# Performance work log

Hardware: AMD Instinct MI355X
Metric: run time of the kernel (lower is better)

The kernel has to match this reference:

```python
import jax, jax.numpy as jnp
import numpy as np

B, L, D, H = 2, 2048, 2048, 16
HD = D // H          # head_dim = 128
LAT = HD // 4        # latent_dim = 32


def setup_inputs() -> dict:
    key = jax.random.key(0)
    ks = jax.random.split(key, 16)
    def w(k, shape, fan_in):
        return jax.random.normal(k, shape, jnp.float32) / np.float32(np.sqrt(fan_in))
    x = jax.random.normal(ks[0], (B, L, D), jnp.float32)
    # RoPE frequencies, stored as (cos, sin) pairs: [L, HD//2, 2]
    inv_freq = 1.0 / (10000.0 ** (np.arange(0, HD, 2, dtype=np.float32) / HD))
    ang = np.outer(np.arange(L, dtype=np.float32), inv_freq)
    freqs_cis = jnp.stack([jnp.asarray(np.cos(ang)), jnp.asarray(np.sin(ang))], axis=-1)
    return dict(
        x=x, freqs_cis=freqs_cis,
        Wq=w(ks[1], (D, D), D), bq=jnp.zeros((D,), jnp.float32),
        Wk=w(ks[2], (D, D), D), bk=jnp.zeros((D,), jnp.float32),
        Wv=w(ks[3], (D, D), D), bv=jnp.zeros((D,), jnp.float32),
        Wqc=w(ks[4], (LAT, HD), HD), bqc=jnp.zeros((LAT,), jnp.float32),
        Wkc=w(ks[5], (LAT, HD), HD), bkc=jnp.zeros((LAT,), jnp.float32),
        Wvc=w(ks[6], (LAT, HD), HD), bvc=jnp.zeros((LAT,), jnp.float32),
        Wd=w(ks[7], (HD, LAT), LAT), bd=jnp.zeros((HD,), jnp.float32),
        Wo=w(ks[8], (D, D), D), bo=jnp.zeros((D,), jnp.float32),
    )


def _rope(t, freqs_cis):
    # t: [B,H,L,HD]; freqs_cis: [L, HD//2, 2] (cos, sin)
    tp = t.reshape(t.shape[:-1] + (HD // 2, 2))
    a, b = tp[..., 0], tp[..., 1]
    cr = freqs_cis[:, :, 0]  # [L, HD//2]
    ci = freqs_cis[:, :, 1]
    ra = a * cr - b * ci
    rb = a * ci + b * cr
    return jnp.stack([ra, rb], axis=-1).reshape(t.shape)


def reference(x, freqs_cis, Wq, bq, Wk, bk, Wv, bv, Wqc, bqc, Wkc, bkc, Wvc, bvc, Wd, bd, Wo, bo):
    Bx, Lx, Dx = x.shape
    # QKV projections -> [B,H,L,HD]
    def proj(W, bias):
        return (x @ W.T + bias).reshape(Bx, Lx, H, HD).transpose(0, 2, 1, 3)
    q = proj(Wq, bq)
    k = proj(Wk, bk)
    v = proj(Wv, bv)
    q = _rope(q, freqs_cis)
    k = _rope(k, freqs_cis)
    # per-head compression to latent dim: [B,H,L,LAT]
    qc = q @ Wqc.T + bqc
    kc = k @ Wkc.T + bkc
    vc = v @ Wvc.T + bvc
    scores = jnp.einsum('bhie,bhje->bhij', qc, kc) / np.float32(np.sqrt(LAT))
    mask = jnp.triu(jnp.ones((Lx, Lx), bool), 1)  # future positions
    scores = jnp.where(mask, jnp.float32(-jnp.inf), scores)
    probs = jax.nn.softmax(scores, axis=-1)
    attn = jnp.einsum('bhij,bhje->bhie', probs, vc)  # [B,H,L,LAT]
    attn = attn @ Wd.T + bd                          # decompress -> [B,H,L,HD]
    attn = attn.transpose(0, 2, 1, 3).reshape(Bx, Lx, Dx)
    return attn @ Wo.T + bo
```

## Files before the change

kernel.cpp:

```cpp
#include <hip/hip_runtime.h>

typedef __attribute__((ext_vector_type(8))) __bf16 bf16x8;
typedef __attribute__((ext_vector_type(4))) __bf16 bf16x4;
typedef __attribute__((ext_vector_type(4))) float f32x4;
typedef __attribute__((ext_vector_type(16))) float f32x16;

#define LL 2048
#define DD 2048
#define HH 16
#define HDIM 128

__global__ __launch_bounds__(256)
void setup_all(const float* __restrict__ x, const float* __restrict__ Wq,
               const float* __restrict__ Wk, const float* __restrict__ Wqc,
               const float* __restrict__ Wkc,
               const float* __restrict__ Wv, const float* __restrict__ Wvc,
               const float* __restrict__ bv, const float* __restrict__ bvc,
               const float* __restrict__ Wo, const float* __restrict__ Wd,
               const float* __restrict__ bd, const float* __restrict__ bo,
               __bf16* __restrict__ xb, __bf16* __restrict__ Wqb, __bf16* __restrict__ Wkb,
               __bf16* __restrict__ Wqcb, __bf16* __restrict__ Wkcb,
               __bf16* __restrict__ Wveff, float* __restrict__ bveff,
               __bf16* __restrict__ Woeff, float* __restrict__ boeff)
{
    __shared__ float sm[128 * 32];
    const int tid = threadIdx.x;
    const int bid = blockIdx.x;

    if (bid < 16392) {
        size_t i = (size_t)bid * 256 + tid;
        const float* s; __bf16* d; size_t off;
        if (i < 2097152)      { s = x;   d = xb;   off = i; }
        else if (i < 3145728) { s = Wq;  d = Wqb;  off = i - 2097152; }
        else if (i < 4194304) { s = Wk;  d = Wkb;  off = i - 3145728; }
        else if (i < 4195328) { s = Wqc; d = Wqcb; off = i - 4194304; }
        else                  { s = Wkc; d = Wkcb; off = i - 4195328; }
        float4 v = *(const float4*)(s + off * 4);
        bf16x4 o = { (__bf16)v.x, (__bf16)v.y, (__bf16)v.z, (__bf16)v.w };
        *(bf16x4*)(d + off * 4) = o;
        return;
    }
    int idx = bid - 16392;
    if (idx < 512) {
        float (*WvcT)[32] = (float(*)[32])sm;
        const int h = idx >> 5, dc = idx & 31;
        for (int i = tid; i < 4096; i += 256) WvcT[i & 127][i >> 7] = Wvc[i];
        __syncthreads();
        const int d  = dc * 64 + (tid & 63);
        const int o0 = (tid >> 6) * 8;
        float acc[8] = {};
        for (int jj = 0; jj < 128; ++jj) {
            const float w = Wv[(size_t)(h * 128 + jj) * 2048 + d];
            #pragma unroll
            for (int o = 0; o < 8; ++o) acc[o] += WvcT[jj][o0 + o] * w;
        }
        #pragma unroll
        for (int o = 0; o < 8; ++o)
            Wveff[(size_t)(h * 32 + o0 + o) * 2048 + d] = (__bf16)acc[o];
        if (dc == 0 && tid < 32) {
            float s = bvc[tid];
            for (int jj = 0; jj < 128; ++jj) s += WvcT[jj][tid] * bv[h * 128 + jj];
            bveff[h * 32 + tid] = s;
        }
        return;
    }
    idx -= 512;
    if (idx < 512) {
        float (*WdL)[32] = (float(*)[32])sm;
        const int dc = idx & 31, h = idx >> 5;
        for (int i = tid; i < 4096; i += 256) WdL[i >> 5][i & 31] = Wd[i];
        __syncthreads();
        const int dout = dc * 64 + (tid & 63);
        const int o0   = (tid >> 6) * 8;
        float acc[8] = {};
        const float* wrow = Wo + (size_t)dout * 2048 + h * 128;
        for (int u = 0; u < 128; ++u) {
            const float w = wrow[u];
            #pragma unroll
            for (int o = 0; o < 8; ++o) acc[o] += WdL[u][o0 + o] * w;
        }
        #pragma unroll
        for (int o = 0; o < 8; ++o)
            Woeff[(size_t)dout * 512 + h * 32 + o0 + o] = (__bf16)acc[o];
        return;
    }
    idx -= 512;
    float* bdL = sm;
    if (tid < 128) bdL[tid] = bd[tid];
    __syncthreads();
    const int d  = idx * 32 + (tid >> 3);
    const int s0 = (tid & 7) * 64;
    float s = 0.f;
    const float* wrow = Wo + (size_t)d * 2048 + s0 * 4;
    for (int c4 = 0; c4 < 64; ++c4) {
        float4 wv = *(const float4*)(wrow + c4 * 4);
        const int cb = ((s0 + c4) * 4) & 127;
        s += wv.x * bdL[cb] + wv.y * bdL[cb + 1] + wv.z * bdL[cb + 2] + wv.w * bdL[cb + 3];
    }
    #pragma unroll
    for (int off = 4; off; off >>= 1) s += __shfl_down(s, off, 8);
    if ((tid & 7) == 0) boeff[d] = bo[d] + s;
}

typedef unsigned int u32;
typedef const __attribute__((address_space(1))) u32* gp_t;
typedef __attribute__((address_space(3))) u32* lp_t;
__device__ __forceinline__ void gload16(const __bf16* g, __bf16* l)
{
    __builtin_amdgcn_global_load_lds((gp_t)(const void*)g, (lp_t)(void*)l, 16, 0, 0);
}

#define MF16(a, b, c) __builtin_amdgcn_mfma_f32_16x16x32_bf16(a, b, c, 0, 0, 0)

__global__ __launch_bounds__(256, 2)
void gemm_qkv(const __bf16* __restrict__ A,
              const __bf16* __restrict__ Wq, const __bf16* __restrict__ Wk,
              const __bf16* __restrict__ Wveff,
              const float* __restrict__ bq, const float* __restrict__ bk,
              const float* __restrict__ bveff,
              const __bf16* __restrict__ Wqcb, const __bf16* __restrict__ Wkcb,
              const float* __restrict__ bqc, const float* __restrict__ bkc,
              const float* __restrict__ fc,
              __bf16* __restrict__ qc, __bf16* __restrict__ kc, __bf16* __restrict__ vt)
{
    __shared__ __bf16 lds[3][12288];

    const int bid = blockIdx.x;
    const int xcd = bid & 7;
    const int j   = bid >> 3;
    const int bx  = j >> 2;
    const int byl = j & 3;
    const int by  = xcd * 4 + byl;
    const int m0  = by * 128;
    const int which = (bx >= 16) ? 2 : (bx >> 3);
    const int n0  = (which == 2) ? (bx - 16) * 256 : (bx & 7) * 256;
    const __bf16* W = which == 0 ? Wq : which == 1 ? Wk : Wveff;

    const int tid  = threadIdx.x;
    const int wid  = tid >> 6;
    const int lane = tid & 63;
    const int wr   = wid >> 1;
    const int wc   = wid & 1;
    const int l15  = lane & 15;
    const int l4   = lane >> 4;
    const int swz  = (l4 ^ (l15 & 3) ^ ((l15 >> 2) & 3)) * 8;

    const int srl  = lane >> 2;
    const int scol = ((lane & 3) ^ (srl & 3) ^ ((srl >> 2) & 3)) * 8;
    const __bf16* gA0 = A + (size_t)(m0 + wid * 32 + srl) * 2048 + scol;
    const __bf16* gB0 = W + (size_t)(n0 + wid * 64 + srl) * 2048 + scol;

    #define STAGE(bb, kk)                                                \
    {   __bf16* dA = &lds[bb][wid * 1024];                               \
        __bf16* dB = &lds[bb][4096 + wid * 2048];                        \
        gload16(gA0 + (kk), dA);                                         \
        gload16(gA0 + (size_t)16 * 2048 + (kk), dA + 512);               \
        gload16(gB0 + (kk), dB);                                         \
        gload16(gB0 + (size_t)16 * 2048 + (kk), dB + 512);               \
        gload16(gB0 + (size_t)32 * 2048 + (kk), dB + 1024);              \
        gload16(gB0 + (size_t)48 * 2048 + (kk), dB + 1536);              \
    }
    #define RD_A(bb, mf) (*(const bf16x8*)&lds[bb][(wr * 64 + (mf) * 16 + l15) * 32 + swz])
    #define RD_B(bb, nf) (*(const bf16x8*)&lds[bb][4096 + (wc * 128 + (nf) * 16 + l15) * 32 + swz])

    f32x4 acc[4][8] = {};

    STAGE(0, 0) STAGE(1, 32)
    asm volatile("s_waitcnt vmcnt(6)" ::: "memory");
    __builtin_amdgcn_s_barrier();

    #define TB(RB, SB, VM, DOST, kk)                                          \
    {                                                                         \
        bf16x8 fa[4], fb[8];                                                  \
        fa[0] = RD_A(RB, 0); fa[1] = RD_A(RB, 1);                             \
        fa[2] = RD_A(RB, 2); fa[3] = RD_A(RB, 3);                             \
        fb[0] = RD_B(RB, 0); fb[1] = RD_B(RB, 1);                             \
        fb[2] = RD_B(RB, 2); fb[3] = RD_B(RB, 3);                             \
        fb[4] = RD_B(RB, 4); fb[5] = RD_B(RB, 5);                             \
        fb[6] = RD_B(RB, 6); fb[7] = RD_B(RB, 7);                             \
        if (DOST) STAGE(SB, kk)                                               \
        asm volatile("s_waitcnt lgkmcnt(0)" ::: "memory");                    \
        __builtin_amdgcn_sched_barrier(0);                                    \
        __builtin_amdgcn_s_setprio(1);                                        \
        _Pragma("unroll")                                                     \
        for (int mf = 0; mf < 4; ++mf)                                        \
            _Pragma("unroll")                                                 \
            for (int nf = 0; nf < 8; ++nf)                                    \
                acc[mf][nf] = MF16(fa[mf], fb[nf], acc[mf][nf]);              \
        __builtin_amdgcn_s_setprio(0);                                        \
        asm volatile("s_waitcnt vmcnt(" VM ")" ::: "memory");                 \
        __builtin_amdgcn_s_barrier();                                         \
    }

    for (int tt = 0; tt < 60; tt += 3) {
        const int kk = (tt + 2) * 32;
        TB(0, 2, "6", true, kk)
        TB(1, 0, "6", true, kk + 32)
        TB(2, 1, "6", true, kk + 64)
    }
    TB(0, 2, "6", true, 62 * 32)
    TB(1, 0, "6", true, 63 * 32)
    TB(2, 0, "0", false, 0)
    TB(0, 0, "0", false, 0)
    #undef TB
    #undef STAGE
    #undef RD_A
    #undef RD_B

    if (which < 2) {
        __bf16* qt = &lds[0][0];
        const float* bb_ = which ? bk : bq;
        const __bf16* Wb = which ? Wkcb : Wqcb;
        const float*  bs = which ? bkc : bqc;
        const int o   = lane & 31;
        const int hi  = lane >> 5;
        const int b   = m0 >> 11;
        const int l0b = m0 & 2047;
        const int lrow = wid * 32 + o;
        const int l    = l0b + lrow;
        const float* fcr = fc + (size_t)l * 128;
        const float QSCALE = 0.17677669529663689f * 1.44269504088896340f;
        __bf16* outp = which ? kc : qc;

        bf16x8 wf[8];
        #pragma unroll
        for (int ks = 0; ks < 8; ++ks)
            wf[ks] = *(const bf16x8*)(Wb + o * 128 + ks * 16 + hi * 8);

        #pragma unroll
        for (int half = 0; half < 2; ++half) {
            if (wc == half) {
                #pragma unroll
                for (int nf = 0; nf < 8; ++nf) {
                    const int col = nf * 16 + l15;
                    const float bv = bb_[n0 + half * 128 + col];
                    #pragma unroll
                    for (int mf = 0; mf < 4; ++mf) {
                        const int row0 = wr * 64 + mf * 16 + l4 * 4;
                        #pragma unroll
                        for (int rr = 0; rr < 4; ++rr)
                            qt[(row0 + rr) * 136 + col] = (__bf16)(acc[mf][nf][rr] + bv);
                    }
                }
            }
            __syncthreads();

            const int h = (n0 >> 7) + half;
            f32x16 C = {};
            #pragma unroll
            for (int ks = 0; ks < 8; ++ks) {
                bf16x8 af = *(const bf16x8*)&qt[lrow * 136 + ks * 16 + hi * 8];
                const float4 cA = *(const float4*)(fcr + (ks * 8 + hi * 4) * 2);
                const float4 cB = *(const float4*)(fcr + (ks * 8 + hi * 4) * 2 + 4);
                float a, b_;
                a = (float)af[0]; b_ = (float)af[1];
                af[0] = (__bf16)(a * cA.x - b_ * cA.y); af[1] = (__bf16)(a * cA.y + b_ * cA.x);
                a = (float)af[2]; b_ = (float)af[3];
                af[2] = (__bf16)(a * cA.z - b_ * cA.w); af[3] = (__bf16)(a * cA.w + b_ * cA.z);
                a = (float)af[4]; b_ = (float)af[5];
                af[4] = (__bf16)(a * cB.x - b_ * cB.y); af[5] = (__bf16)(a * cB.y + b_ * cB.x);
                a = (float)af[6]; b_ = (float)af[7];
                af[6] = (__bf16)(a * cB.z - b_ * cB.w); af[7] = (__bf16)(a * cB.w + b_ * cB.z);
                C = __builtin_amdgcn_mfma_f32_32x32x16_bf16(af, wf[ks], C, 0, 0, 0);
            }

            const float bias = bs[o];
            const size_t g0row = (size_t)(b * 16 + h) * 2048 + l0b + wid * 32;
            #pragma unroll
            for (int r = 0; r < 16; ++r) {
                const int ro = (r & 3) + 8 * (r >> 2) + 4 * hi;
                float v = C[r] + bias;
                if (which == 0) v *= QSCALE;
                outp[(g0row + ro) * 32 + o] = (__bf16)v;
            }
            __syncthreads();
        }
    } else {
        #pragma unroll
        for (int nf = 0; nf < 8; ++nf) {
            const int ncol = n0 + wc * 128 + nf * 16 + l15;
            const float bv = bveff[ncol];
            const int hh = ncol >> 5, oo = ncol & 31;
            #pragma unroll
            for (int mf = 0; mf < 4; ++mf) {
                const int row0 = m0 + wr * 64 + mf * 16 + l4 * 4;
                const int b = row0 >> 11, l0 = row0 & 2047;
                bf16x4 pk = { (__bf16)(acc[mf][nf][0] + bv), (__bf16)(acc[mf][nf][1] + bv),
                              (__bf16)(acc[mf][nf][2] + bv), (__bf16)(acc[mf][nf][3] + bv) };
                *(bf16x4*)(vt + ((size_t)((b * 16 + hh) * 32 + oo)) * 2048 + l0) = pk;
            }
        }
    }
}

__global__ __launch_bounds__(256, 3)
void gemm_ao(const __bf16* __restrict__ ao, const __bf16* __restrict__ Woeff,
             const float* __restrict__ boeff, float* __restrict__ out)
{
    __shared__ __bf16 lds[3][2][4096];
    const int bid = blockIdx.x;
    const int x   = bid & 7;
    const int jj  = bid >> 3;
    const int bx  = x * 2 + (jj & 1);
    const int by  = jj >> 1;
    const int m0  = by * 128;
    const int n0  = bx * 128;

    const int tid  = threadIdx.x;
    const int wid  = tid >> 6;
    const int lane = tid & 63;
    const int wr   = wid >> 1;
    const int wc   = wid & 1;
    const int l15  = lane & 15;
    const int l4   = lane >> 4;
    const int swz  = (l4 ^ (l15 & 3) ^ ((l15 >> 2) & 3)) * 8;

    const int srl  = lane >> 2;
    const int scol = ((lane & 3) ^ (srl & 3) ^ ((srl >> 2) & 3)) * 8;
    const int r0   = m0 + wid * 32 + srl;
    const int b0   = r0 >> 11, li0 = r0 & 2047;
    const __bf16* gA0 = ao + ((size_t)(b0 << 4) * 2048 + li0) * 32 + scol;
    const __bf16* gA1 = ao + ((size_t)(b0 << 4) * 2048 + li0 + 16) * 32 + scol;
    const __bf16* gB0 = Woeff + (size_t)(n0 + wid * 32 + srl) * 512 + scol;

    #define STAGE(bb, kk)                                                     \
    {   __bf16* dA = &lds[bb][0][wid * 1024];                                 \
        __bf16* dB = &lds[bb][1][wid * 1024];                                 \
        const size_t ka = (size_t)((kk) >> 5) * 65536;                        \
        gload16(gA0 + ka, dA);                                                \
        gload16(gA1 + ka, dA + 512);                                          \
        gload16(gB0 + (kk), dB);                                              \
        gload16(gB0 + (size_t)16 * 512 + (kk), dB + 512);                     \
    }
    #define RD_A(bb, mf) (*(const bf16x8*)&lds[bb][0][(wr * 64 + (mf) * 16 + l15) * 32 + swz])
    #define RD_B(bb, nf) (*(const bf16x8*)&lds[bb][1][(wc * 64 + (nf) * 16 + l15) * 32 + swz])

    f32x4 acc[4][4] = {};

    STAGE(0, 0) STAGE(1, 32)
    asm volatile("s_waitcnt vmcnt(4)" ::: "memory");
    __builtin_amdgcn_s_barrier();

    #define TB(RB, SB, VM, DOST, kk)                                          \
    {                                                                         \
        bf16x8 fa[4], fb[4];                                                  \
        fa[0] = RD_A(RB, 0); fa[1] = RD_A(RB, 1);                             \
        fa[2] = RD_A(RB, 2); fa[3] = RD_A(RB, 3);                             \
        fb[0] = RD_B(RB, 0); fb[1] = RD_B(RB, 1);                             \
        fb[2] = RD_B(RB, 2); fb[3] = RD_B(RB, 3);                             \
        if (DOST) STAGE(SB, kk)                                               \
        asm volatile("s_waitcnt lgkmcnt(0)" ::: "memory");                    \
        __builtin_amdgcn_sched_barrier(0);                                    \
        __builtin_amdgcn_s_setprio(1);                                        \
        _Pragma("unroll")                                                     \
        for (int mf = 0; mf < 4; ++mf)                                        \
            _Pragma("unroll")                                                 \
            for (int nf = 0; nf < 4; ++nf)                                    \
                acc[mf][nf] = MF16(fa[mf], fb[nf], acc[mf][nf]);              \
        __builtin_amdgcn_s_setprio(0);                                        \
        asm volatile("s_waitcnt vmcnt(" VM ")" ::: "memory");                 \
        __builtin_amdgcn_s_barrier();                                         \
    }

    for (int tt = 0; tt < 12; tt += 3) {
        const int kk = (tt + 2) * 32;
        TB(0, 2, "4", true, kk)
        TB(1, 0, "4", true, kk + 32)
        TB(2, 1, "4", true, kk + 64)
    }
    TB(0, 2, "4", true, 14 * 32)
    TB(1, 0, "4", true, 15 * 32)
    TB(2, 0, "0", false, 0)
    TB(0, 0, "0", false, 0)
    #undef TB
    #undef STAGE
    #undef RD_A
    #undef RD_B

    #pragma unroll
    for (int nf = 0; nf < 4; ++nf) {
        const int col = n0 + wc * 64 + nf * 16 + l15;
        const float bv = boeff[col];
        #pragma unroll
        for (int mf = 0; mf < 4; ++mf) {
            const int row0 = m0 + wr * 64 + mf * 16 + l4 * 4;
            #pragma unroll
            for (int rr = 0; rr < 4; ++rr)
                out[(size_t)(row0 + rr) * 2048 + col] = acc[mf][nf][rr] + bv;
        }
    }
}

__device__ __forceinline__ unsigned pkbf2(float a, float b)
{
    union { __bf16 h[2]; unsigned u; } x;
    x.h[0] = (__bf16)a; x.h[1] = (__bf16)b;
    return x.u;
}

#if __has_builtin(__builtin_amdgcn_permlane32_swap)
typedef unsigned int uint2v __attribute__((ext_vector_type(2)));
__device__ __forceinline__ void plswap(unsigned a, unsigned b, unsigned& w_lo, unsigned& w_hi, int)
{
    uint2v r = __builtin_amdgcn_permlane32_swap(a, b, false, false);
    w_lo = r[0]; w_hi = r[1];
}
#else
__device__ __forceinline__ void plswap(unsigned a, unsigned b, unsigned& w_lo, unsigned& w_hi, int hi)
{
    unsigned ax = (unsigned)__shfl_xor((int)a, 32);
    unsigned bx = (unsigned)__shfl_xor((int)b, 32);
    w_lo = hi ? bx : a;
    w_hi = hi ? b  : ax;
}
#endif

__global__ __launch_bounds__(256)
void attn_part(const __bf16* __restrict__ qc, const __bf16* __restrict__ kc,
               const __bf16* __restrict__ vt,
               float* __restrict__ pl, float* __restrict__ po)
{
    const int id  = blockIdx.x * 4 + (threadIdx.x >> 6);
    const int bhl = id & 7;
    const int c   = id >> 3;
    const int bhh = c / 160;
    const int lin = c - bhh * 160;
    int s, ci;
    if (lin < 16)      { s = lin; ci = 0; }
    else if (lin < 48) { int q = lin - 16; s = 16 + (q >> 1); ci = q & 1; }
    else if (lin < 96) { int q = lin - 48; int d = q / 3; s = 32 + d; ci = q - d * 3; }
    else               { int q = lin - 96; s = 48 + (q >> 2); ci = q & 3; }
    const int bh = bhh * 8 + bhl;

    const int lane = threadIdx.x & 63;
    const int qcol = lane & 31;
    const int hi   = lane >> 5;

    const __bf16* qbase = qc + ((size_t)bh * LL + (size_t)s * 32) * 32;
    const __bf16* kbase = kc + (size_t)bh * LL * 32;
    const __bf16* vbase = vt + (size_t)bh * 32 * LL;

    const bf16x8 qf0 = *(const bf16x8*)(qbase + qcol * 32 + hi * 8);
    const bf16x8 qf1 = *(const bf16x8*)(qbase + qcol * 32 + 16 + hi * 8);

    const float M2 = 16.0f;
    float lsum = 0.f;
    f32x16 O = {};

    const int t0 = ci * 16;
    const int t1 = min(s, t0 + 15);

    const __bf16* krow = kbase + (size_t)(t0 * 32 + qcol) * 32 + hi * 8;
    const __bf16* vrow = vbase + (size_t)qcol * LL + t0 * 32 + hi * 8;
    bf16x8 kc0 = *(const bf16x8*)(krow);
    bf16x8 kc1 = *(const bf16x8*)(krow + 16);
    bf16x8 vc0 = *(const bf16x8*)(vrow);
    bf16x8 vc1 = *(const bf16x8*)(vrow + 16);

    for (int t = t0; t <= t1; ++t) {
        const int tn = (t < t1) ? t + 1 : t;
        const __bf16* krn = kbase + (size_t)(tn * 32 + qcol) * 32 + hi * 8;
        const __bf16* vrn = vbase + (size_t)qcol * LL + tn * 32 + hi * 8;
        bf16x8 kn0 = *(const bf16x8*)(krn);
        bf16x8 kn1 = *(const bf16x8*)(krn + 16);
        bf16x8 vn0 = *(const bf16x8*)(vrn);
        bf16x8 vn1 = *(const bf16x8*)(vrn + 16);

        f32x16 S = {};
        S = __builtin_amdgcn_mfma_f32_32x32x16_bf16(kc0, qf0, S, 0, 0, 0);
        S = __builtin_amdgcn_mfma_f32_32x32x16_bf16(kc1, qf1, S, 0, 0, 0);

        if (t == s) {
            #pragma unroll
            for (int r = 0; r < 16; ++r) {
                const int kl = (r & 3) + 8 * (r >> 2) + 4 * hi;
                if (kl > qcol) S[r] = -1e30f;
            }
        }
        float p[16];
        #pragma unroll
        for (int r = 0; r < 16; ++r) { p[r] = exp2f(S[r] - M2); lsum += p[r]; }

        unsigned w[8];
        #pragma unroll
        for (int i = 0; i < 8; ++i) w[i] = pkbf2(p[2 * i], p[2 * i + 1]);
        union PF { unsigned u[4]; bf16x8 v; } pf1, pf2;
        plswap(w[0], w[2], pf1.u[0], pf1.u[2], hi);
        plswap(w[1], w[3], pf1.u[1], pf1.u[3], hi);
        plswap(w[4], w[6], pf2.u[0], pf2.u[2], hi);
        plswap(w[5], w[7], pf2.u[1], pf2.u[3], hi);

        O = __builtin_amdgcn_mfma_f32_32x32x16_bf16(vc0, pf1.v, O, 0, 0, 0);
        O = __builtin_amdgcn_mfma_f32_32x32x16_bf16(vc1, pf2.v, O, 0, 0, 0);

        kc0 = kn0; kc1 = kn1; vc0 = vn0; vc1 = vn1;
    }

    const float L = lsum + __shfl_xor(lsum, 32);
    const size_t g = (size_t)bh * LL + (size_t)s * 32 + qcol;
    const size_t slot = g * 4 + ci;
    if (hi == 0) pl[slot] = L;
    float* pp = po + slot * 32;
    #pragma unroll
    for (int g4 = 0; g4 < 4; ++g4) {
        float4 v = { O[g4 * 4 + 0], O[g4 * 4 + 1], O[g4 * 4 + 2], O[g4 * 4 + 3] };
        *(float4*)(pp + g4 * 8 + 4 * hi) = v;
    }
}

__global__ __launch_bounds__(256)
void attn_comb(const float* __restrict__ pl, const float* __restrict__ po,
               __bf16* __restrict__ ao)
{
    const int g = blockIdx.x * 256 + threadIdx.x;
    const int i = g & (LL - 1);
    const int nch = (i >> 9) + 1;
    float L = 0.f;
    float o[32] = {};
    for (int c = 0; c < nch; ++c) {
        L += pl[(size_t)g * 4 + c];
        const float* pp = po + ((size_t)g * 4 + c) * 32;
        #pragma unroll
        for (int d4 = 0; d4 < 8; ++d4) {
            float4 v = *(const float4*)(pp + d4 * 4);
            o[d4*4+0] += v.x; o[d4*4+1] += v.y;
            o[d4*4+2] += v.z; o[d4*4+3] += v.w;
        }
    }
    const float inv = 1.f / L;
    #pragma unroll
    for (int d8 = 0; d8 < 4; ++d8) {
        bf16x8 v;
        #pragma unroll
        for (int jj = 0; jj < 8; ++jj) v[jj] = (__bf16)(o[d8 * 8 + jj] * inv);
        *(bf16x8*)(ao + (size_t)g * 32 + d8 * 8) = v;
    }
}

extern "C" void kernel_launch(void* const* d_in, const int* in_sizes, int n_in,
                              void* d_out, int out_size, void* d_ws, size_t ws_size,
                              hipStream_t stream)
{
    const float* x   = (const float*)d_in[0];
    const float* fc  = (const float*)d_in[1];
    const float* Wq  = (const float*)d_in[2];
    const float* bq  = (const float*)d_in[3];
    const float* Wk  = (const float*)d_in[4];
    const float* bk  = (const float*)d_in[5];
    const float* Wv  = (const float*)d_in[6];
    const float* bv  = (const float*)d_in[7];
    const float* Wqc = (const float*)d_in[8];
    const float* bqc = (const float*)d_in[9];
    const float* Wkc = (const float*)d_in[10];
    const float* bkc = (const float*)d_in[11];
    const float* Wvc = (const float*)d_in[12];
    const float* bvc = (const float*)d_in[13];
    const float* Wd  = (const float*)d_in[14];
    const float* bd  = (const float*)d_in[15];
    const float* Wo  = (const float*)d_in[16];
    const float* bo  = (const float*)d_in[17];
    float* out = (float*)d_out;

    const size_t MB = 1048576;
    char* w = (char*)d_ws;
    __bf16* xb    = (__bf16*)(w);
    __bf16* Wqb   = (__bf16*)(w + 16 * MB);
    __bf16* Wkb   = (__bf16*)(w + 24 * MB);
    __bf16* Wveff = (__bf16*)(w + 32 * MB);
    __bf16* qcbf  = (__bf16*)(w + 66 * MB);
    __bf16* kcbf  = (__bf16*)(w + 70 * MB);
    __bf16* vtbf  = (__bf16*)(w + 74 * MB);
    __bf16* aobf  = (__bf16*)(w + 78 * MB);
    __bf16* Wqcb  = (__bf16*)(w + 82 * MB);
    __bf16* Wkcb  = (__bf16*)(w + 82 * MB + 8192);
    __bf16* Woeff = (__bf16*)(w + 83 * MB);
    float*  boeff = (float*)(w + 85 * MB);
    float*  bveff = (float*)(w + 85 * MB + 8192);

    float* po = (float*)d_ws;
    float* pl = (float*)(w + 32 * MB);

    if (ws_size < (size_t)90 * MB) return;

    setup_all<<<17480, 256, 0, stream>>>(x, Wq, Wk, Wqc, Wkc, Wv, Wvc, bv, bvc,
                                         Wo, Wd, bd, bo,
                                         xb, Wqb, Wkb, Wqcb, Wkcb,
                                         Wveff, bveff, Woeff, boeff);

    gemm_qkv<<<576, 256, 0, stream>>>(xb, Wqb, Wkb, Wveff, bq, bk, bveff,
                                      Wqcb, Wkcb, bqc, bkc, fc, qcbf, kcbf, vtbf);

    attn_part<<<1280, 256, 0, stream>>>(qcbf, kcbf, vtbf, pl, po);
    attn_comb<<<256, 256, 0, stream>>>(pl, po, aobf);

    gemm_ao<<<512, 256, 0, stream>>>(aobf, Woeff, boeff, out);
}
```

Before: 217.5 us.

## Halve attention split-K chunk size and store partial outputs in bf16

Each causal attention work item now covers at most 8 key tiles instead of 16, so each query tile is split into up to 8 chunks. A closed-form triangular index decode with a sqrt estimate maps the linear work id to (query tile, chunk), and the grid grows to 2304 blocks. This is meant to raise wave count and shorten the longest per-wave loop, improving load balance across the GPU. Partial outputs are written as bf16 instead of fp32 to cut the write and read traffic this adds. The combine kernel must now sum up to 8 partials, and the unnormalized bf16 partials lose some precision.

```diff
diff --git a/kernel.cpp b/kernel.cpp
--- a/kernel.cpp
+++ b/kernel.cpp
@@ -418,19 +418,21 @@
 __global__ __launch_bounds__(256)
 void attn_part(const __bf16* __restrict__ qc, const __bf16* __restrict__ kc,
                const __bf16* __restrict__ vt,
-               float* __restrict__ pl, float* __restrict__ po)
+               float* __restrict__ pl, __bf16* __restrict__ po)
 {
     const int id  = blockIdx.x * 4 + (threadIdx.x >> 6);
     const int bhl = id & 7;
     const int c   = id >> 3;
-    const int bhh = c / 160;
-    const int lin = c - bhh * 160;
-    int s, ci;
-    if (lin < 16)      { s = lin; ci = 0; }
-    else if (lin < 48) { int q = lin - 16; s = 16 + (q >> 1); ci = q & 1; }
-    else if (lin < 96) { int q = lin - 48; int d = q / 3; s = 32 + d; ci = q - d * 3; }
-    else               { int q = lin - 96; s = 48 + (q >> 2); ci = q & 3; }
-    const int bh = bhh * 8 + bhl;
+    const int bhh = c / 288;
+    const int lin = c - bhh * 288;
+    int g = (int)((sqrtf((float)lin + 1.0f) - 1.0f) * 0.5f);
+    while (4 * (g + 1) * (g + 2) <= lin) ++g;
+    while (4 * g * (g + 1) > lin) --g;
+    const int rem = lin - 4 * g * (g + 1);
+    const int sq  = rem / (g + 1);
+    const int s   = 8 * g + sq;
+    const int ci  = rem - sq * (g + 1);
+    const int bh  = bhh * 8 + bhl;
 
     const int lane = threadIdx.x & 63;
     const int qcol = lane & 31;
@@ -447,8 +449,8 @@
     float lsum = 0.f;
     f32x16 O = {};
 
-    const int t0 = ci * 16;
-    const int t1 = min(s, t0 + 15);
+    const int t0 = ci * 8;
+    const int t1 = min(s, t0 + 7);
 
     const __bf16* krow = kbase + (size_t)(t0 * 32 + qcol) * 32 + hi * 8;
     const __bf16* vrow = vbase + (size_t)qcol * LL + t0 * 32 + hi * 8;
@@ -497,34 +499,35 @@
     }
 
     const float L = lsum + __shfl_xor(lsum, 32);
-    const size_t g = (size_t)bh * LL + (size_t)s * 32 + qcol;
-    const size_t slot = g * 4 + ci;
+    const size_t gq = (size_t)bh * LL + (size_t)s * 32 + qcol;
+    const size_t slot = gq * 8 + ci;
     if (hi == 0) pl[slot] = L;
-    float* pp = po + slot * 32;
+    __bf16* pp = po + slot * 32;
     #pragma unroll
     for (int g4 = 0; g4 < 4; ++g4) {
-        float4 v = { O[g4 * 4 + 0], O[g4 * 4 + 1], O[g4 * 4 + 2], O[g4 * 4 + 3] };
-        *(float4*)(pp + g4 * 8 + 4 * hi) = v;
+        bf16x4 pk = { (__bf16)O[g4 * 4 + 0], (__bf16)O[g4 * 4 + 1],
+                      (__bf16)O[g4 * 4 + 2], (__bf16)O[g4 * 4 + 3] };
+        *(bf16x4*)(pp + g4 * 8 + 4 * hi) = pk;
     }
 }
 
 __global__ __launch_bounds__(256)
-void attn_comb(const float* __restrict__ pl, const float* __restrict__ po,
+void attn_comb(const float* __restrict__ pl, const __bf16* __restrict__ po,
                __bf16* __restrict__ ao)
 {
     const int g = blockIdx.x * 256 + threadIdx.x;
     const int i = g & (LL - 1);
-    const int nch = (i >> 9) + 1;
+    const int nch = (i >> 8) + 1;
     float L = 0.f;
     float o[32] = {};
     for (int c = 0; c < nch; ++c) {
-        L += pl[(size_t)g * 4 + c];
-        const float* pp = po + ((size_t)g * 4 + c) * 32;
-        #pragma unroll
-        for (int d4 = 0; d4 < 8; ++d4) {
-            float4 v = *(const float4*)(pp + d4 * 4);
-            o[d4*4+0] += v.x; o[d4*4+1] += v.y;
-            o[d4*4+2] += v.z; o[d4*4+3] += v.w;
+        L += pl[(size_t)g * 8 + c];
+        const __bf16* pp = po + ((size_t)g * 8 + c) * 32;
+        #pragma unroll
+        for (int d8 = 0; d8 < 4; ++d8) {
+            bf16x8 v = *(const bf16x8*)(pp + d8 * 8);
+            #pragma unroll
+            for (int jj = 0; jj < 8; ++jj) o[d8 * 8 + jj] += (float)v[jj];
         }
     }
     const float inv = 1.f / L;
@@ -577,8 +580,8 @@
     float*  boeff = (float*)(w + 85 * MB);
     float*  bveff = (float*)(w + 85 * MB + 8192);
 
-    float* po = (float*)d_ws;
-    float* pl = (float*)(w + 32 * MB);
+    __bf16* po = (__bf16*)d_ws;
+    float*  pl = (float*)(w + 32 * MB);
 
     if (ws_size < (size_t)90 * MB) return;
 
@@ -590,7 +593,7 @@
     gemm_qkv<<<576, 256, 0, stream>>>(xb, Wqb, Wkb, Wveff, bq, bk, bveff,
                                       Wqcb, Wkcb, bqc, bkc, fc, qcbf, kcbf, vtbf);
 
-    attn_part<<<1280, 256, 0, stream>>>(qcbf, kcbf, vtbf, pl, po);
+    attn_part<<<2304, 256, 0, stream>>>(qcbf, kcbf, vtbf, pl, po);
     attn_comb<<<256, 256, 0, stream>>>(pl, po, aobf);
 
     gemm_ao<<<512, 256, 0, stream>>>(aobf, Woeff, boeff, out);
```

Result: no change. 216.6 us (-0.4%).
